# Performance work log

Hardware: AMD Instinct MI355X
Metric: run time of the kernel (lower is better)

Reference implementation:

```python
import jax, jax.numpy as jnp
import numpy as np

RADII = np.array([0.5, 1.0, 1.5, 2.0], dtype=np.float32)
SIGMA = 0.5          # gaussian radial-function width (= radius spacing)
EPS = 1e-8
N_SH = 9             # real spherical harmonics up to l=2
N_BASIS = len(RADII) * N_SH


def real_sh_l2(u):
    """Real spherical harmonics l=0,1,2 of unit vectors u[..., 3] -> [..., 9]."""
    x, y, z = u[..., 0], u[..., 1], u[..., 2]
    one = jnp.ones_like(x)
    return jnp.stack([
        0.28209479 * one,
        0.48860251 * x, 0.48860251 * y, 0.48860251 * z,
        1.09254843 * x * y,
        1.09254843 * y * z,
        0.31539157 * (3.0 * z * z - 1.0),
        1.09254843 * x * z,
        0.54627421 * (x * x - y * y),
    ], axis=-1)


def setup_inputs() -> dict:
    key = jax.random.key(0)
    k1, k2, k3, k4, k5 = jax.random.split(key, 5)
    n, c_in, d_out, b, a = 4, 32, 32, 8192, 32
    inp = jax.random.normal(k1, (n, c_in, b), jnp.float32)
    coords = jax.random.uniform(k2, (n, b, 3), jnp.float32) * 4.0
    neighbors = jax.random.randint(k3, (n, b, a), 0, b)
    relative_mask = jax.random.uniform(k4, (n, b, a), jnp.float32)
    W = jax.random.normal(k5, (d_out, c_in, N_BASIS), jnp.float32) / np.sqrt(c_in * N_BASIS)
    return {"input": inp, "coords": coords, "relative_mask": relative_mask,
            "W": W, "neighbors": neighbors}


def reference(input, coords, relative_mask, W, neighbors):
    n, c, b = input.shape
    idx_n = jnp.arange(n)[:, None, None]                     # [n,1,1]
    # neighbor difference matrix: coords[neighbors] - coords  -> [n,b,a,3]
    neigh_xyz = coords[idx_n, neighbors]
    diff = neigh_xyz - coords[:, :, None, :]
    r = jnp.linalg.norm(diff, axis=-1)                       # [n,b,a]
    u = diff / (r[..., None] + EPS)
    Y = real_sh_l2(u)                                        # [n,b,a,9]
    radii = jnp.asarray(RADII)
    rb = jnp.exp(-((r[..., None] - radii) / SIGMA) ** 2)     # [n,b,a,4]
    basis = (rb[..., :, None] * Y[..., None, :]).reshape(r.shape + (-1,))  # [n,b,a,36]
    # neighbor feature matrix: input[n, :, neighbors[n,b,a]] -> [n,b,a,c]
    feat = input[idx_n, :, neighbors]
    # relative_mask multiplies k over (n,b,a) == masking gathered features
    feat = feat * relative_mask[..., None]
    # fused form of: k[d,c,n,b,a] = sum_k basis[n,b,a,k] W[d,c,k];
    # out[n,d,b] = sum_{c,a} feat[n,b,a,c] * k[d,c,n,b,a]
    M = jnp.einsum('nbac,nbak->nbck', feat, basis)           # [n,b,c,36]
    return jnp.einsum('nbck,dck->ndb', M, W)
```

## Files before the change

kernel.cpp:

```cpp
#include <hip/hip_runtime.h>
#include <hip/hip_bf16.h>


typedef _Float16 f16x8 __attribute__((ext_vector_type(8)));
typedef _Float16 f16x4 __attribute__((ext_vector_type(4)));
typedef __fp16   h16x2 __attribute__((ext_vector_type(2)));
typedef float    f32x4 __attribute__((ext_vector_type(4)));
typedef unsigned int u32;

__device__ __forceinline__ u32 pk16(float a, float b) {
    union { h16x2 v; u32 u; } cv;
    cv.v = __builtin_amdgcn_cvt_pkrtz(a, b);
    return cv.u;
}
__device__ __forceinline__ unsigned short f16bits(float v) {
    const _Float16 hv = (_Float16)v;
    return __builtin_bit_cast(unsigned short, hv);
}

#define BAS_STRIDE 44

__device__ __forceinline__ void geom(float dx, float dy, float dz, float msk, int h_,
                                     float Y[9], float& rbA, float& rbB) {
    const float r   = sqrtf(dx * dx + dy * dy + dz * dz);
    const float inv = 1.0f / (r + 1e-8f);
    const float x = dx * inv, y = dy * inv, z = dz * inv;
    Y[0] = 0.28209479f;
    Y[1] = 0.48860251f * x;
    Y[2] = 0.48860251f * y;
    Y[3] = 0.48860251f * z;
    Y[4] = 1.09254843f * x * y;
    Y[5] = 1.09254843f * y * z;
    Y[6] = 0.31539157f * (3.0f * z * z - 1.0f);
    Y[7] = 1.09254843f * x * z;
    Y[8] = 0.54627421f * (x * x - y * y);
    const float t0 = (r - 0.5f) * 2.0f;
    const float t1 = (r - 1.0f) * 2.0f;
    const float t2 = (r - 1.5f) * 2.0f;
    const float t3 = (r - 2.0f) * 2.0f;
    const float rb0 = __expf(-t0 * t0) * msk;
    const float rb1 = __expf(-t1 * t1) * msk;
    const float rb2 = __expf(-t2 * t2) * msk;
    const float rb3 = __expf(-t3 * t3) * msk;
    rbA = h_ ? rb2 : rb0;
    rbB = h_ ? rb3 : rb1;
}

__global__ __launch_bounds__(256) void prep_kernel(
    const float* __restrict__ inp, const float* __restrict__ W,
    unsigned short* __restrict__ inp_t16, unsigned short* __restrict__ Wfrag)
{
    if (blockIdx.x < 1024) {
        __shared__ float T[32][33];
        const int n  = blockIdx.x >> 8;
        const int b0 = (blockIdx.x & 255) << 5;
        const int bx = threadIdx.x & 31;
        const int cy = threadIdx.x >> 5;
        #pragma unroll
        for (int r = 0; r < 4; ++r) {
            const int cc = cy + r * 8;
            T[bx][cc] = inp[((n << 5) + cc) * 8192 + b0 + bx];
        }
        __syncthreads();
        #pragma unroll
        for (int r = 0; r < 4; ++r) {
            const int by = cy + r * 8;
            inp_t16[((n << 13) + b0 + by) * 32 + bx] = f16bits(T[by][bx]);
        }
    } else {
        const int t = (blockIdx.x - 1024) * 256 + threadIdx.x;
        if (t < 36 * 2 * 64 * 8) {
            const int j  = t & 7;
            const int l  = (t >> 3) & 63;
            const int dt = (t >> 9) & 1;
            const int kt = t >> 10;
            const int d  = dt * 16 + (l & 15);
            const int c  = ((l >> 4) << 3) + j;
            Wfrag[t] = f16bits(W[d * 1152 + c * 36 + kt]);
        }
    }
}

__global__ __launch_bounds__(512, 4) void se3_main(
    const unsigned short* __restrict__ inp_t16, const float* __restrict__ coords,
    const float* __restrict__ rmask, const int* __restrict__ neigh,
    const unsigned short* __restrict__ Wfrag, float* __restrict__ out)
{
    __shared__ __align__(16) unsigned short Mb_s[36 * 580];
    __shared__ __align__(16) unsigned short bas[8][37 * BAS_STRIDE];
    __shared__ unsigned short idxs[16][32];
    __shared__ __align__(16) float Cp[8 * 64 * 4];

    const int tid  = threadIdx.x;
    const int lane = tid & 63;
    const int w    = tid >> 6;
    const int l15  = lane & 15;
    const int q    = lane >> 4;
    const int a_   = lane & 31;
    const int h_   = lane >> 5;

    const int blk = blockIdx.x;
    const int n_  = (blk & 7) >> 1;
    const int pos = ((blk >> 3) << 1) | (blk & 1);
    const int b0  = pos << 4;
    const int gp0 = (n_ << 13) | b0;
    const int nbase_pt = n_ << 13;
    const unsigned short* __restrict__ inp_n = inp_t16 + ((size_t)n_ << 18);

    unsigned short* basw = &bas[w][0];

    const int dt  = w >> 2;
    const int seg = w & 3;
    const int kt0 = seg * 9;
    f16x8 wf0, wf1, wf2, wf3, wf4, wf5, wf6, wf7, wf8;
    {
        const unsigned short* wb = &Wfrag[((size_t)((kt0 * 2 + dt) * 64 + lane)) << 3];
        wf0 = *(const f16x8*)(wb + 0 * 1024);
        wf1 = *(const f16x8*)(wb + 1 * 1024);
        wf2 = *(const f16x8*)(wb + 2 * 1024);
        wf3 = *(const f16x8*)(wb + 3 * 1024);
        wf4 = *(const f16x8*)(wb + 4 * 1024);
        wf5 = *(const f16x8*)(wb + 5 * 1024);
        wf6 = *(const f16x8*)(wb + 6 * 1024);
        wf7 = *(const f16x8*)(wb + 7 * 1024);
        wf8 = *(const f16x8*)(wb + 8 * 1024);
    }

    const int ph0 = 2 * l15;
    const int ph1 = (l15 < 2) ? (32 + 2 * l15) : (2 * l15 - 3);
    const int ph2 = (l15 < 4) ? (29 + 2 * l15) : 36;
    const int offB0 = ph0 * BAS_STRIDE + (q << 3);
    const int offB1 = ph1 * BAS_STRIDE + (q << 3);
    const int offB2 = ph2 * BAS_STRIDE + (q << 3);

    const int pA = w << 1, pB = pA | 1;
    const int gpA = gp0 + pA, gpB = gp0 + pB;

    const int   idxA = neigh[(gpA << 5) | a_];
    const int   idxB = neigh[(gpB << 5) | a_];
    const float mskA = rmask[(gpA << 5) | a_];
    const float mskB = rmask[(gpB << 5) | a_];
    const float cxA = coords[gpA * 3 + 0], cyA = coords[gpA * 3 + 1], czA = coords[gpA * 3 + 2];
    const float cxB = coords[gpB * 3 + 0], cyB = coords[gpB * 3 + 1], czB = coords[gpB * 3 + 2];
    if (lane < 32) {
        idxs[pA][a_] = (unsigned short)idxA;
        idxs[pB][a_] = (unsigned short)idxB;
    }
    const int nbA = (nbase_pt + idxA) * 3;
    const int nbB = (nbase_pt + idxB) * 3;
    const float dxA = coords[nbA + 0] - cxA, dyA = coords[nbA + 1] - cyA, dzA = coords[nbA + 2] - czA;
    const float dxB = coords[nbB + 0] - cxB, dyB = coords[nbB + 1] - cyB, dzB = coords[nbB + 2] - czB;

    u32 fA0[8], fA1[8], fB0[8], fB1[8];
    #pragma unroll
    for (int j = 0; j < 8; ++j) {
        const int ri = idxs[pA][(q << 3) + j];
        const unsigned short* rp = inp_n + (((unsigned)ri) << 5) + l15;
        fA0[j] = rp[0];
        fA1[j] = rp[16];
    }
    #pragma unroll
    for (int j = 0; j < 8; ++j) {
        const int ri = idxs[pB][(q << 3) + j];
        const unsigned short* rp = inp_n + (((unsigned)ri) << 5) + l15;
        fB0[j] = rp[0];
        fB1[j] = rp[16];
    }

    float YA[9], YB[9], rbA_A, rbB_A, rbA_B, rbB_B;
    geom(dxA, dyA, dzA, mskA, h_, YA, rbA_A, rbB_A);
    geom(dxB, dyB, dzB, mskB, h_, YB, rbA_B, rbB_B);

    #pragma unroll
    for (int t = 0; t < 18; ++t) {
        const float v = (t < 9) ? rbA_A * YA[t] : rbB_A * YA[t - 9];
        basw[(2 * t + h_) * BAS_STRIDE + a_] = f16bits(v);
    }

    f16x4 blo, bhi;
    blo = *(const f16x4*)&basw[offB0]; bhi = *(const f16x4*)&basw[offB0 + 4];
    const f16x8 BfA0 = __builtin_shufflevector(blo, bhi, 0, 1, 2, 3, 4, 5, 6, 7);
    blo = *(const f16x4*)&basw[offB1]; bhi = *(const f16x4*)&basw[offB1 + 4];
    const f16x8 BfA1 = __builtin_shufflevector(blo, bhi, 0, 1, 2, 3, 4, 5, 6, 7);
    blo = *(const f16x4*)&basw[offB2]; bhi = *(const f16x4*)&basw[offB2 + 4];
    const f16x8 BfA2 = __builtin_shufflevector(blo, bhi, 0, 1, 2, 3, 4, 5, 6, 7);

    union { f16x8 v; u32 u[4]; } afA0, afA1, afB0, afB1;
    #pragma unroll
    for (int j4 = 0; j4 < 4; ++j4) {
        afA0.u[j4] = fA0[2 * j4] | (fA0[2 * j4 + 1] << 16);
        afA1.u[j4] = fA1[2 * j4] | (fA1[2 * j4 + 1] << 16);
    }
    const f32x4 z4 = {0.0f, 0.0f, 0.0f, 0.0f};
    f32x4 DA00 = __builtin_amdgcn_mfma_f32_16x16x32_f16(afA0.v, BfA0, z4, 0, 0, 0);
    f32x4 DA01 = __builtin_amdgcn_mfma_f32_16x16x32_f16(afA0.v, BfA1, z4, 0, 0, 0);
    f32x4 DA02 = __builtin_amdgcn_mfma_f32_16x16x32_f16(afA0.v, BfA2, z4, 0, 0, 0);
    f32x4 DA10 = __builtin_amdgcn_mfma_f32_16x16x32_f16(afA1.v, BfA0, z4, 0, 0, 0);
    f32x4 DA11 = __builtin_amdgcn_mfma_f32_16x16x32_f16(afA1.v, BfA1, z4, 0, 0, 0);
    f32x4 DA12 = __builtin_amdgcn_mfma_f32_16x16x32_f16(afA1.v, BfA2, z4, 0, 0, 0);

    #pragma unroll
    for (int t = 0; t < 18; ++t) {
        const float v = (t < 9) ? rbA_B * YB[t] : rbB_B * YB[t - 9];
        basw[(2 * t + h_) * BAS_STRIDE + a_] = f16bits(v);
    }
    blo = *(const f16x4*)&basw[offB0]; bhi = *(const f16x4*)&basw[offB0 + 4];
    const f16x8 BfB0 = __builtin_shufflevector(blo, bhi, 0, 1, 2, 3, 4, 5, 6, 7);
    blo = *(const f16x4*)&basw[offB1]; bhi = *(const f16x4*)&basw[offB1 + 4];
    const f16x8 BfB1 = __builtin_shufflevector(blo, bhi, 0, 1, 2, 3, 4, 5, 6, 7);
    blo = *(const f16x4*)&basw[offB2]; bhi = *(const f16x4*)&basw[offB2 + 4];
    const f16x8 BfB2 = __builtin_shufflevector(blo, bhi, 0, 1, 2, 3, 4, 5, 6, 7);

    #pragma unroll
    for (int j4 = 0; j4 < 4; ++j4) {
        afB0.u[j4] = fB0[2 * j4] | (fB0[2 * j4 + 1] << 16);
        afB1.u[j4] = fB1[2 * j4] | (fB1[2 * j4 + 1] << 16);
    }
    f32x4 DB00 = __builtin_amdgcn_mfma_f32_16x16x32_f16(afB0.v, BfB0, z4, 0, 0, 0);
    f32x4 DB01 = __builtin_amdgcn_mfma_f32_16x16x32_f16(afB0.v, BfB1, z4, 0, 0, 0);
    f32x4 DB02 = __builtin_amdgcn_mfma_f32_16x16x32_f16(afB0.v, BfB2, z4, 0, 0, 0);
    f32x4 DB10 = __builtin_amdgcn_mfma_f32_16x16x32_f16(afB1.v, BfB0, z4, 0, 0, 0);
    f32x4 DB11 = __builtin_amdgcn_mfma_f32_16x16x32_f16(afB1.v, BfB1, z4, 0, 0, 0);
    f32x4 DB12 = __builtin_amdgcn_mfma_f32_16x16x32_f16(afB1.v, BfB2, z4, 0, 0, 0);

    {
        const int rowpA = pA * 36 + (q << 2);
        const int a0 = l15 * 580 + rowpA;
        const int a1 = (16 + l15) * 580 + rowpA;
        *(u32*)&Mb_s[a0]      = pk16(DA00[0], DA00[1]);
        *(u32*)&Mb_s[a0 + 2]  = pk16(DA00[2], DA00[3]);
        *(u32*)&Mb_s[a0 + 16] = pk16(DA10[0], DA10[1]);
        *(u32*)&Mb_s[a0 + 18] = pk16(DA10[2], DA10[3]);
        *(u32*)&Mb_s[a1]      = pk16(DA01[0], DA01[1]);
        *(u32*)&Mb_s[a1 + 2]  = pk16(DA01[2], DA01[3]);
        *(u32*)&Mb_s[a1 + 16] = pk16(DA11[0], DA11[1]);
        *(u32*)&Mb_s[a1 + 18] = pk16(DA11[2], DA11[3]);
        const int rowpB = pB * 36 + (q << 2);
        const int c0 = l15 * 580 + rowpB;
        const int c1 = (16 + l15) * 580 + rowpB;
        *(u32*)&Mb_s[c0]      = pk16(DB00[0], DB00[1]);
        *(u32*)&Mb_s[c0 + 2]  = pk16(DB00[2], DB00[3]);
        *(u32*)&Mb_s[c0 + 16] = pk16(DB10[0], DB10[1]);
        *(u32*)&Mb_s[c0 + 18] = pk16(DB10[2], DB10[3]);
        *(u32*)&Mb_s[c1]      = pk16(DB01[0], DB01[1]);
        *(u32*)&Mb_s[c1 + 2]  = pk16(DB01[2], DB01[3]);
        *(u32*)&Mb_s[c1 + 16] = pk16(DB11[0], DB11[1]);
        *(u32*)&Mb_s[c1 + 18] = pk16(DB11[2], DB11[3]);
        if (l15 < 4) {
            const int a2 = (32 + l15) * 580 + rowpA;
            *(u32*)&Mb_s[a2]      = pk16(DA02[0], DA02[1]);
            *(u32*)&Mb_s[a2 + 2]  = pk16(DA02[2], DA02[3]);
            *(u32*)&Mb_s[a2 + 16] = pk16(DA12[0], DA12[1]);
            *(u32*)&Mb_s[a2 + 18] = pk16(DA12[2], DA12[3]);
            const int c2 = (32 + l15) * 580 + rowpB;
            *(u32*)&Mb_s[c2]      = pk16(DB02[0], DB02[1]);
            *(u32*)&Mb_s[c2 + 2]  = pk16(DB02[2], DB02[3]);
            *(u32*)&Mb_s[c2 + 16] = pk16(DB12[0], DB12[1]);
            *(u32*)&Mb_s[c2 + 18] = pk16(DB12[2], DB12[3]);
        }
    }
    __syncthreads();

    {
        f32x4 acc2 = {0.0f, 0.0f, 0.0f, 0.0f};
        #define P2_STEP(I, WF)                                                       \
        {                                                                            \
            const int mbase = (kt0 + I) * 580 + l15 * 36 + (q << 3);                 \
            const f16x4 mlo = *(const f16x4*)&Mb_s[mbase];                           \
            const f16x4 mhi = *(const f16x4*)&Mb_s[mbase + 4];                       \
            const f16x8 bf  = __builtin_shufflevector(mlo, mhi, 0,1,2,3,4,5,6,7);    \
            acc2 = __builtin_amdgcn_mfma_f32_16x16x32_f16(WF, bf, acc2, 0, 0, 0);    \
        }
        P2_STEP(0, wf0) P2_STEP(1, wf1) P2_STEP(2, wf2)
        P2_STEP(3, wf3) P2_STEP(4, wf4) P2_STEP(5, wf5)
        P2_STEP(6, wf6) P2_STEP(7, wf7) P2_STEP(8, wf8)
        #undef P2_STEP
        *(f32x4*)&Cp[(w * 64 + lane) * 4] = acc2;
    }
    __syncthreads();

    if (w < 2) {
        const int dt2 = w;
        f32x4 s = *(const f32x4*)&Cp[((dt2 * 4 + 0) * 64 + lane) * 4];
        #pragma unroll
        for (int rphase = 1; rphase < 4; ++rphase) {
            const f32x4 t = *(const f32x4*)&Cp[((dt2 * 4 + rphase) * 64 + lane) * 4];
            s[0] += t[0]; s[1] += t[1]; s[2] += t[2]; s[3] += t[3];
        }
        const int drow = dt2 * 16 + (lane >> 4) * 4;
        const int col  = b0 + (lane & 15);
        #pragma unroll
        for (int rr = 0; rr < 4; ++rr) {
            out[(((n_ << 5) + drow + rr) << 13) + col] = s[rr];
        }
    }
}

extern "C" void kernel_launch(void* const* d_in, const int* in_sizes, int n_in,
                              void* d_out, int out_size, void* d_ws, size_t ws_size,
                              hipStream_t stream)
{
    const float* inp    = (const float*)d_in[0];
    const float* coords = (const float*)d_in[1];
    const float* rmask  = (const float*)d_in[2];
    const float* W      = (const float*)d_in[3];
    const int*   neigh  = (const int*)d_in[4];
    float*       outp   = (float*)d_out;

    unsigned short* inp_t16 = (unsigned short*)d_ws;
    unsigned short* Wfrag   = (unsigned short*)((char*)d_ws + (2u << 20));

    prep_kernel<<<1168, 256, 0, stream>>>(inp, W, inp_t16, Wfrag);
    se3_main<<<2048, 512, 0, stream>>>(inp_t16, coords, rmask, neigh, Wfrag, outp);
}
```

Measured before the change: 90.90 us.

## Pad coords to float4, interleave channel pairs, simplify geometry math

The prep kernel now writes a float4-padded copy of coords and stores the fp16 input with channels c and c+16 interleaved. This lets the main kernel fetch each neighbor's coordinates with one 16-byte load and both channel halves with one 32-bit gather, split afterward by v_perm. The geometry routine uses rsqrt instead of sqrt plus a divide, and evaluates only the two Gaussians each lane needs instead of four. The aim is fewer scattered gather instructions and less ALU work, in exchange for 128 extra prep blocks and extra workspace traffic.

Measured after the change: 88.69 us. 1.02x faster.

```diff
diff --git a/kernel.cpp b/kernel.cpp
--- a/kernel.cpp
+++ b/kernel.cpp
@@ -22,8 +22,9 @@
 
 __device__ __forceinline__ void geom(float dx, float dy, float dz, float msk, int h_,
                                      float Y[9], float& rbA, float& rbB) {
-    const float r   = sqrtf(dx * dx + dy * dy + dz * dz);
-    const float inv = 1.0f / (r + 1e-8f);
+    const float d2  = dx * dx + dy * dy + dz * dz;
+    const float inv = rsqrtf(d2 + 1e-16f);
+    const float r   = d2 * inv;
     const float x = dx * inv, y = dy * inv, z = dz * inv;
     Y[0] = 0.28209479f;
     Y[1] = 0.48860251f * x;
@@ -34,21 +35,17 @@
     Y[6] = 0.31539157f * (3.0f * z * z - 1.0f);
     Y[7] = 1.09254843f * x * z;
     Y[8] = 0.54627421f * (x * x - y * y);
-    const float t0 = (r - 0.5f) * 2.0f;
-    const float t1 = (r - 1.0f) * 2.0f;
-    const float t2 = (r - 1.5f) * 2.0f;
-    const float t3 = (r - 2.0f) * 2.0f;
-    const float rb0 = __expf(-t0 * t0) * msk;
-    const float rb1 = __expf(-t1 * t1) * msk;
-    const float rb2 = __expf(-t2 * t2) * msk;
-    const float rb3 = __expf(-t3 * t3) * msk;
-    rbA = h_ ? rb2 : rb0;
-    rbB = h_ ? rb3 : rb1;
+    const float sA = r - (h_ ? 1.5f : 0.5f);
+    const float sB = r - (h_ ? 2.0f : 1.0f);
+    rbA = __expf(sA * sA * -4.0f) * msk;
+    rbB = __expf(sB * sB * -4.0f) * msk;
 }
 
 __global__ __launch_bounds__(256) void prep_kernel(
     const float* __restrict__ inp, const float* __restrict__ W,
-    unsigned short* __restrict__ inp_t16, unsigned short* __restrict__ Wfrag)
+    const float* __restrict__ coords,
+    unsigned short* __restrict__ inp_t16, unsigned short* __restrict__ Wfrag,
+    float* __restrict__ coords4)
 {
     if (blockIdx.x < 1024) {
         __shared__ float T[32][33];
@@ -62,12 +59,13 @@
             T[bx][cc] = inp[((n << 5) + cc) * 8192 + b0 + bx];
         }
         __syncthreads();
+        const int cpos = ((bx & 15) << 1) | (bx >> 4);
         #pragma unroll
         for (int r = 0; r < 4; ++r) {
             const int by = cy + r * 8;
-            inp_t16[((n << 13) + b0 + by) * 32 + bx] = f16bits(T[by][bx]);
-        }
-    } else {
+            inp_t16[((n << 13) + b0 + by) * 32 + cpos] = f16bits(T[by][bx]);
+        }
+    } else if (blockIdx.x < 1168) {
         const int t = (blockIdx.x - 1024) * 256 + threadIdx.x;
         if (t < 36 * 2 * 64 * 8) {
             const int j  = t & 7;
@@ -78,11 +76,19 @@
             const int c  = ((l >> 4) << 3) + j;
             Wfrag[t] = f16bits(W[d * 1152 + c * 36 + kt]);
         }
+    } else {
+        const int t = (blockIdx.x - 1168) * 256 + threadIdx.x;
+        f32x4 v;
+        v[0] = coords[3 * t + 0];
+        v[1] = coords[3 * t + 1];
+        v[2] = coords[3 * t + 2];
+        v[3] = 0.0f;
+        *(f32x4*)(coords4 + ((size_t)t << 2)) = v;
     }
 }
 
 __global__ __launch_bounds__(512, 4) void se3_main(
-    const unsigned short* __restrict__ inp_t16, const float* __restrict__ coords,
+    const unsigned short* __restrict__ inp_t16, const float* __restrict__ coords4,
     const float* __restrict__ rmask, const int* __restrict__ neigh,
     const unsigned short* __restrict__ Wfrag, float* __restrict__ out)
 {
@@ -140,31 +146,27 @@
     const int   idxB = neigh[(gpB << 5) | a_];
     const float mskA = rmask[(gpA << 5) | a_];
     const float mskB = rmask[(gpB << 5) | a_];
-    const float cxA = coords[gpA * 3 + 0], cyA = coords[gpA * 3 + 1], czA = coords[gpA * 3 + 2];
-    const float cxB = coords[gpB * 3 + 0], cyB = coords[gpB * 3 + 1], czB = coords[gpB * 3 + 2];
+    const f32x4 cA4 = *(const f32x4*)(coords4 + ((size_t)gpA << 2));
+    const f32x4 cB4 = *(const f32x4*)(coords4 + ((size_t)gpB << 2));
     if (lane < 32) {
         idxs[pA][a_] = (unsigned short)idxA;
         idxs[pB][a_] = (unsigned short)idxB;
     }
-    const int nbA = (nbase_pt + idxA) * 3;
-    const int nbB = (nbase_pt + idxB) * 3;
-    const float dxA = coords[nbA + 0] - cxA, dyA = coords[nbA + 1] - cyA, dzA = coords[nbA + 2] - czA;
-    const float dxB = coords[nbB + 0] - cxB, dyB = coords[nbB + 1] - cyB, dzB = coords[nbB + 2] - czB;
-
-    u32 fA0[8], fA1[8], fB0[8], fB1[8];
+    const f32x4 nA4 = *(const f32x4*)(coords4 + ((size_t)(nbase_pt + idxA) << 2));
+    const f32x4 nB4 = *(const f32x4*)(coords4 + ((size_t)(nbase_pt + idxB) << 2));
+    const float dxA = nA4[0] - cA4[0], dyA = nA4[1] - cA4[1], dzA = nA4[2] - cA4[2];
+    const float dxB = nB4[0] - cB4[0], dyB = nB4[1] - cB4[1], dzB = nB4[2] - cB4[2];
+
+    u32 gA[8], gB[8];
     #pragma unroll
     for (int j = 0; j < 8; ++j) {
         const int ri = idxs[pA][(q << 3) + j];
-        const unsigned short* rp = inp_n + (((unsigned)ri) << 5) + l15;
-        fA0[j] = rp[0];
-        fA1[j] = rp[16];
+        gA[j] = *(const u32*)(inp_n + (((unsigned)ri) << 5) + (l15 << 1));
     }
     #pragma unroll
     for (int j = 0; j < 8; ++j) {
         const int ri = idxs[pB][(q << 3) + j];
-        const unsigned short* rp = inp_n + (((unsigned)ri) << 5) + l15;
-        fB0[j] = rp[0];
-        fB1[j] = rp[16];
+        gB[j] = *(const u32*)(inp_n + (((unsigned)ri) << 5) + (l15 << 1));
     }
 
     float YA[9], YB[9], rbA_A, rbB_A, rbA_B, rbB_B;
@@ -188,8 +190,8 @@
     union { f16x8 v; u32 u[4]; } afA0, afA1, afB0, afB1;
     #pragma unroll
     for (int j4 = 0; j4 < 4; ++j4) {
-        afA0.u[j4] = fA0[2 * j4] | (fA0[2 * j4 + 1] << 16);
-        afA1.u[j4] = fA1[2 * j4] | (fA1[2 * j4 + 1] << 16);
+        afA0.u[j4] = __builtin_amdgcn_perm(gA[2 * j4 + 1], gA[2 * j4], 0x05040100u);
+        afA1.u[j4] = __builtin_amdgcn_perm(gA[2 * j4 + 1], gA[2 * j4], 0x07060302u);
     }
     const f32x4 z4 = {0.0f, 0.0f, 0.0f, 0.0f};
     f32x4 DA00 = __builtin_amdgcn_mfma_f32_16x16x32_f16(afA0.v, BfA0, z4, 0, 0, 0);
@@ -213,8 +215,8 @@
 
     #pragma unroll
     for (int j4 = 0; j4 < 4; ++j4) {
-        afB0.u[j4] = fB0[2 * j4] | (fB0[2 * j4 + 1] << 16);
-        afB1.u[j4] = fB1[2 * j4] | (fB1[2 * j4 + 1] << 16);
+        afB0.u[j4] = __builtin_amdgcn_perm(gB[2 * j4 + 1], gB[2 * j4], 0x05040100u);
+        afB1.u[j4] = __builtin_amdgcn_perm(gB[2 * j4 + 1], gB[2 * j4], 0x07060302u);
     }
     f32x4 DB00 = __builtin_amdgcn_mfma_f32_16x16x32_f16(afB0.v, BfB0, z4, 0, 0, 0);
     f32x4 DB01 = __builtin_amdgcn_mfma_f32_16x16x32_f16(afB0.v, BfB1, z4, 0, 0, 0);
@@ -309,7 +311,8 @@
 
     unsigned short* inp_t16 = (unsigned short*)d_ws;
     unsigned short* Wfrag   = (unsigned short*)((char*)d_ws + (2u << 20));
-
-    prep_kernel<<<1168, 256, 0, stream>>>(inp, W, inp_t16, Wfrag);
-    se3_main<<<2048, 512, 0, stream>>>(inp_t16, coords, rmask, neigh, Wfrag, outp);
-}
+    float*          coords4 = (float*)((char*)d_ws + (4u << 20));
+
+    prep_kernel<<<1296, 256, 0, stream>>>(inp, W, coords, inp_t16, Wfrag, coords4);
+    se3_main<<<2048, 512, 0, stream>>>(inp_t16, coords4, rmask, neigh, Wfrag, outp);
+}
```
